# Kernel tuning notes

Hardware: AMD Instinct MI355X
Metric: run time of the kernel (lower is better)

The kernel has to match this reference:

```python
import jax, jax.numpy as jnp
import numpy as np

N_NODES = 100000
N_EDGES = 1600000
IN_DIM = 128
HID = 128
OUT = 128
NUM_GRAPHS = 2048


def setup_inputs() -> dict:
    key = jax.random.key(0)
    ks = jax.random.split(key, 10)
    x = jax.random.normal(ks[0], (N_NODES, IN_DIM), dtype=jnp.float32)
    edge_index = jax.random.randint(ks[1], (2, N_EDGES), 0, N_NODES, dtype=jnp.int32)
    graph_index = jnp.sort(jax.random.randint(ks[2], (N_NODES,), 0, NUM_GRAPHS, dtype=jnp.int32))
    def glorot(k, fi, fo):
        lim = jnp.sqrt(6.0 / (fi + fo)).astype(jnp.float32)
        return jax.random.uniform(k, (fi, fo), jnp.float32, -lim, lim)
    return {
        "x": x,
        "edge_index": edge_index,
        "graph_index": graph_index,
        "num_graphs": NUM_GRAPHS,
        "W1": glorot(ks[3], IN_DIM, HID), "b1": jnp.zeros((HID,), jnp.float32),
        "W2": glorot(ks[4], HID, HID),    "b2": jnp.zeros((HID,), jnp.float32),
        "W3": glorot(ks[5], HID, OUT),    "b3": jnp.zeros((OUT,), jnp.float32),
    }


def _gcn_layer(x, src, dst, norm, W, b, n_nodes):
    # transform first (cheap GEMM), then normalized gather-scatter aggregation
    h = x @ W                              # [N, F]
    msg = h[src] * norm[:, None]           # [E+N, F] gather + scale
    out = jax.ops.segment_sum(msg, dst, num_segments=n_nodes)  # scatter-add
    return out + b


def reference(x, edge_index, graph_index, num_graphs, W1, b1, W2, b2, W3, b3):
    n = x.shape[0]
    # add self-loops (PyG GCNConv default)
    loops = jnp.arange(n, dtype=edge_index.dtype)
    src = jnp.concatenate([edge_index[0], loops])
    dst = jnp.concatenate([edge_index[1], loops])
    # symmetric normalization D^-1/2 (A+I) D^-1/2, degree = in-degree incl. self-loop
    deg = jax.ops.segment_sum(jnp.ones_like(src, dtype=x.dtype), dst, num_segments=n)
    dinv = jax.lax.rsqrt(jnp.maximum(deg, 1.0))
    norm = dinv[src] * dinv[dst]
    # 3 conv layers + ReLU (dropout = identity at inference)
    h = jax.nn.relu(_gcn_layer(x, src, dst, norm, W1, b1, n))
    h = jax.nn.relu(_gcn_layer(h, src, dst, norm, W2, b2, n))
    h = jax.nn.relu(_gcn_layer(h, src, dst, norm, W3, b3, n))
    # global mean / max pooling per graph
    gsum = jax.ops.segment_sum(h, graph_index, num_segments=num_graphs)
    cnt = jax.ops.segment_sum(jnp.ones((n,), h.dtype), graph_index, num_segments=num_graphs)
    gmean = gsum / jnp.maximum(cnt, 1.0)[:, None]
    gmax = jax.ops.segment_max(h, graph_index, num_segments=num_graphs)
    return jnp.concatenate([gmean, gmax], axis=-1)
```

## Files before the change

### kernel.cpp

```cpp
#include <hip/hip_runtime.h>
#include <hip/hip_bf16.h>
#include <stdint.h>

#define N_NODES   100000
#define N_EDGES   1600000
#define FDIM      128
#define NUM_GR    2048
#define CSR_CAP   64

#define NBKT      391
#define BKT_CAP   4864
#define TILE      4096
#define LBIN_CAP  16
#define LBIN_STR  17

typedef __attribute__((ext_vector_type(8))) short short8;
typedef __attribute__((ext_vector_type(4))) float f32x4;

__device__ __forceinline__ uint32_t pk2(float a, float b) {
    __hip_bfloat16 x = __float2bfloat16(a), y = __float2bfloat16(b);
    uint16_t ux = *reinterpret_cast<uint16_t*>(&x);
    uint16_t uy = *reinterpret_cast<uint16_t*>(&y);
    return (uint32_t)ux | ((uint32_t)uy << 16);
}

__device__ __forceinline__ float bflo(uint32_t u) { return __uint_as_float(u << 16); }
__device__ __forceinline__ float bfhi(uint32_t u) { return __uint_as_float(u & 0xFFFF0000u); }

__device__ __forceinline__ short8 pack8(float4 u0, float4 u1) {
    union { uint32_t u[4]; short8 s; } cv;
    cv.u[0] = pk2(u0.x, u0.y);
    cv.u[1] = pk2(u0.z, u0.w);
    cv.u[2] = pk2(u1.x, u1.y);
    cv.u[3] = pk2(u1.z, u1.w);
    return cv.s;
}

__device__ __forceinline__ int lower_bound_dev(const int* a, int n, int key) {
    int lo = 0, hi = n;
    while (lo < hi) {
        int m = (lo + hi) >> 1;
        if (a[m] < key) lo = m + 1; else hi = m;
    }
    return lo;
}


__global__ __launch_bounds__(256, 4) void k_fused1(
        const float* __restrict__ x, const float* __restrict__ W1,
        __hip_bfloat16* __restrict__ C, int n, int gGemm,
        const int* __restrict__ src, const int* __restrict__ dst,
        int* __restrict__ bkt_cnt, int* __restrict__ bkt, int E, int gA,
        const float* __restrict__ W2, const float* __restrict__ W3,
        __hip_bfloat16* __restrict__ wt,
        const int* __restrict__ gidx, float* __restrict__ gscale) {
    __shared__ uint32_t smem[8192];
    const int b = blockIdx.x;
    const int tid = threadIdx.x;

    if (b >= gGemm + gA + 128) {
        int g = (b - (gGemm + gA + 128)) * 256 + tid;
        if (g < NUM_GR) {
            int lo = lower_bound_dev(gidx, n, g);
            int hi = lower_bound_dev(gidx, n, g + 1);
            gscale[g] = 1.f / (float)max(hi - lo, 1);
        }
        return;
    }

    if (b >= gGemm + gA) {
        int idx = 16384 + (b - gGemm - gA) * 256 + tid;
        int l = idx >> 14, rem = idx & 16383, c = rem >> 7, k = rem & 127;
        const float* W = (l == 1) ? W2 : W3;
        wt[idx] = __float2bfloat16(W[k * FDIM + c]);
        return;
    }

    if (b >= gGemm) {
        int* binCnt  = (int*)smem;
        int* binBase = (int*)smem + NBKT;
        int* bins    = (int*)smem + 2 * NBKT;
        int bb = b - gGemm;

        for (int i = tid; i < NBKT; i += 256) binCnt[i] = 0;
        __syncthreads();

        int e0 = bb * TILE;
        int e1 = min(E, e0 + TILE);
        for (int e = e0 + tid; e < e1; e += 256) {
            int s = src[e];
            int d = dst[e];
            int bi = d >> 8;
            int rec = ((d & 255) << 17) | s;
            int pos = atomicAdd(&binCnt[bi], 1);
            if (pos < LBIN_CAP) {
                bins[bi * LBIN_STR + pos] = rec;
            } else {
                int gp = atomicAdd(&bkt_cnt[bi], 1);
                if (gp < BKT_CAP) bkt[bi * BKT_CAP + gp] = rec;
            }
        }
        __syncthreads();

        for (int i = tid; i < NBKT; i += 256) {
            int c = min(binCnt[i], LBIN_CAP);
            binBase[i] = (c > 0) ? atomicAdd(&bkt_cnt[i], c) : 0;
        }
        __syncthreads();

        for (int i = tid; i < NBKT * LBIN_CAP; i += 256) {
            int bi = i / LBIN_CAP, sl = i - bi * LBIN_CAP;
            if (sl < min(binCnt[bi], LBIN_CAP)) {
                int gp = binBase[bi] + sl;
                if (gp < BKT_CAP) bkt[bi * BKT_CAP + gp] = bins[bi * LBIN_STR + sl];
            }
        }
        return;
    }

    uint32_t* Wtl = smem;

    const int rowBase = b * 128;

    for (int it = 0; it < 32; ++it) {
        int idx = it * 256 + tid;
        int kp = idx >> 7;
        int c  = idx & 127;
        float w0 = W1[(size_t)(2 * kp) * FDIM + c];
        float w1 = W1[(size_t)(2 * kp + 1) * FDIM + c];
        int word = c * 64 + ((((kp >> 2) ^ (c & 7)) << 2) | (kp & 3));
        Wtl[word] = pk2(w0, w1);
    }
    __syncthreads();

    const int w = tid >> 6;
    const int lane = tid & 63;
    const int r = lane & 15;
    const int q = lane >> 4;

    const int r0c = min(rowBase + w * 32 + r, n - 1);
    const int r1c = min(rowBase + w * 32 + 16 + r, n - 1);

    f32x4 acc[8][2] = {};

#pragma unroll
    for (int kk = 0; kk < 4; ++kk) {
        int co = (kk * 4 + q) * 8;
        const float4* p0 = (const float4*)&x[(size_t)r0c * FDIM + co];
        const float4* p1 = (const float4*)&x[(size_t)r1c * FDIM + co];
        short8 a0 = pack8(p0[0], p0[1]);
        short8 a1 = pack8(p1[0], p1[1]);
        int gr = ((kk * 4 + q) ^ (r & 7)) << 2;
#pragma unroll
        for (int m = 0; m < 8; ++m) {
            short8 bw = *(const short8*)&Wtl[(m * 16 + r) * 64 + gr];
            acc[m][0] = __builtin_amdgcn_mfma_f32_16x16x32_bf16(bw, a0, acc[m][0], 0, 0, 0);
            acc[m][1] = __builtin_amdgcn_mfma_f32_16x16x32_bf16(bw, a1, acc[m][1], 0, 0, 0);
        }
    }

#pragma unroll
    for (int nt = 0; nt < 2; ++nt) {
        int node = rowBase + w * 32 + nt * 16 + r;
        if (node < n) {
#pragma unroll
            for (int m = 0; m < 8; ++m) {
                f32x4 v = acc[m][nt];
                uint2 pv;
                pv.x = pk2(v[0], v[1]);
                pv.y = pk2(v[2], v[3]);
                *(uint2*)&C[(size_t)node * FDIM + m * 16 + q * 4] = pv;
            }
        }
    }
}


__global__ __launch_bounds__(256) void k_csr(const int* __restrict__ bkt_cnt,
                                             const int* __restrict__ bkt,
                                             int* __restrict__ cnt,
                                             float* __restrict__ dinv,
                                             int* __restrict__ csr, int n) {
    __shared__ int lc[64];
    __shared__ int cur[64];
    int b = blockIdx.x;
    int tid = threadIdx.x;
    int bi = b >> 2;
    int qd = b & 3;

    if (b == 0 && tid == 0) dinv[n] = 0.f;

    if (tid < 64) { lc[tid] = 0; cur[tid] = 0; }
    __syncthreads();

    int len = min(bkt_cnt[bi], BKT_CAP);
    const int* recs = bkt + bi * BKT_CAP;

    for (int i = tid; i < len; i += 256) {
        int dl = (recs[i] >> 17) & 255;
        if ((dl >> 6) == qd) atomicAdd(&lc[dl & 63], 1);
    }
    __syncthreads();

    if (tid < 64) {
        int v = (bi << 8) + (qd << 6) + tid;
        if (v < n) {
            int c = lc[tid];
            cnt[v] = c;
            dinv[v] = rsqrtf((float)(c + 1));
        }
    }

    for (int i = tid; i < len; i += 256) {
        int rec = recs[i];
        int dl = (rec >> 17) & 255;
        if ((dl >> 6) == qd) {
            int pos = atomicAdd(&cur[dl & 63], 1);
            if (pos < CSR_CAP)
                csr[(((size_t)(bi << 8) + dl) << 6) + pos] = rec & 0x1FFFF;
        }
    }
}


__global__ __launch_bounds__(256) void k_agg1(const __hip_bfloat16* __restrict__ T,
                                              const int* __restrict__ cnt,
                                              const int* __restrict__ csr,
                                              const float* __restrict__ dinv,
                                              const float* __restrict__ bias,
                                              uint32_t* __restrict__ Hb,
                                              int n) {
    int wid = (blockIdx.x * 256 + threadIdx.x) >> 6;
    int lane = threadIdx.x & 63;
    if (wid >= n) return;
    int v = wid;
    int g   = lane >> 4;
    int s16 = lane & 15;

    const uint4* Tu4 = (const uint4*)T;

    int cv  = min(cnt[v], CSR_CAP);
    int sraw = csr[((size_t)v << 6) + lane];
    int sidx = (lane < cv) ? sraw : ((lane == cv) ? v : n);
    cv += 1;

    float a0 = 0.f, a1 = 0.f, a2 = 0.f, a3 = 0.f;
    float a4 = 0.f, a5 = 0.f, a6 = 0.f, a7 = 0.f;

    int mr = (cv + 15) & ~15;
    for (int j = 0; j < mr; j += 16) {
        uint4 gg[4];
        float wv[4];
#pragma unroll
        for (int t = 0; t < 4; ++t) {
            int it = __shfl(sidx, j + 4 * t + g, 64);
            wv[t] = dinv[it];
            gg[t] = Tu4[(size_t)it * 16 + s16];
        }
#pragma unroll
        for (int t = 0; t < 4; ++t) {
            a0 = fmaf(wv[t], bflo(gg[t].x), a0); a1 = fmaf(wv[t], bfhi(gg[t].x), a1);
            a2 = fmaf(wv[t], bflo(gg[t].y), a2); a3 = fmaf(wv[t], bfhi(gg[t].y), a3);
            a4 = fmaf(wv[t], bflo(gg[t].z), a4); a5 = fmaf(wv[t], bfhi(gg[t].z), a5);
            a6 = fmaf(wv[t], bflo(gg[t].w), a6); a7 = fmaf(wv[t], bfhi(gg[t].w), a7);
        }
    }

    a0 += __shfl_xor(a0, 16, 64); a0 += __shfl_xor(a0, 32, 64);
    a1 += __shfl_xor(a1, 16, 64); a1 += __shfl_xor(a1, 32, 64);
    a2 += __shfl_xor(a2, 16, 64); a2 += __shfl_xor(a2, 32, 64);
    a3 += __shfl_xor(a3, 16, 64); a3 += __shfl_xor(a3, 32, 64);
    a4 += __shfl_xor(a4, 16, 64); a4 += __shfl_xor(a4, 32, 64);
    a5 += __shfl_xor(a5, 16, 64); a5 += __shfl_xor(a5, 32, 64);
    a6 += __shfl_xor(a6, 16, 64); a6 += __shfl_xor(a6, 32, 64);
    a7 += __shfl_xor(a7, 16, 64); a7 += __shfl_xor(a7, 32, 64);

    if (g == 0) {
        float dv = dinv[v];
        float4 bb0 = *(const float4*)&bias[s16 * 8];
        float4 bb1 = *(const float4*)&bias[s16 * 8 + 4];
        float r0 = fmaxf(fmaf(dv, a0, bb0.x), 0.f);
        float r1 = fmaxf(fmaf(dv, a1, bb0.y), 0.f);
        float r2 = fmaxf(fmaf(dv, a2, bb0.z), 0.f);
        float r3 = fmaxf(fmaf(dv, a3, bb0.w), 0.f);
        float r4 = fmaxf(fmaf(dv, a4, bb1.x), 0.f);
        float r5 = fmaxf(fmaf(dv, a5, bb1.y), 0.f);
        float r6 = fmaxf(fmaf(dv, a6, bb1.z), 0.f);
        float r7 = fmaxf(fmaf(dv, a7, bb1.w), 0.f);
        uint4 pv;
        pv.x = pk2(r0, r1);
        pv.y = pk2(r2, r3);
        pv.z = pk2(r4, r5);
        pv.w = pk2(r6, r7);
        *(uint4*)&Hb[(size_t)v * 64 + s16 * 4] = pv;
    }
}


template<int POOL>
__global__ __launch_bounds__(512, 4) void k_aggT(
        const __hip_bfloat16* __restrict__ T,
        const __hip_bfloat16* __restrict__ Wt,
        const int* __restrict__ cnt,
        const int* __restrict__ csr,
        const float* __restrict__ dinv,
        const float* __restrict__ bias,
        uint32_t* __restrict__ Hb,
        const int* __restrict__ gidx,
        const float* __restrict__ gscale,
        float* __restrict__ out,
        int n) {
    __shared__ uint32_t Wl[128 * 64];
    __shared__ uint32_t Hl[32 * 64];

    const int tid = threadIdx.x;

    for (int it = 0; it < 4; ++it) {
        int g = it * 512 + tid;
        int r = g >> 4;
        int seg = g & 15;
        uint4 v = *(const uint4*)&Wt[(size_t)r * FDIM + seg * 8];
        int word = r * 64 + ((seg ^ (r & 7)) << 2);
        *(uint4*)&Wl[word] = v;
    }

    const int w = tid >> 6;
    const int lane = tid & 63;
    const int g = lane >> 4;
    const int s16 = lane & 15;
    const int nodeBase = blockIdx.x * 32;
    const uint4* Tu4 = (const uint4*)T;

    for (int k = 0; k < 4; ++k) {
        int v = nodeBase + w * 4 + k;
        int cv = min(cnt[v], CSR_CAP);
        int sraw = csr[((size_t)v << 6) + lane];
        int sidx = (lane < cv) ? sraw : ((lane == cv) ? v : n);
        cv += 1;

        float a0 = 0.f, a1 = 0.f, a2 = 0.f, a3 = 0.f;
        float a4 = 0.f, a5 = 0.f, a6 = 0.f, a7 = 0.f;

        int mr = (cv + 15) & ~15;
        for (int j = 0; j < mr; j += 16) {
            uint4 gg[4];
            float wv[4];
#pragma unroll
            for (int t = 0; t < 4; ++t) {
                int it = __shfl(sidx, j + 4 * t + g, 64);
                wv[t] = dinv[it];
                gg[t] = Tu4[(size_t)it * 16 + s16];
            }
#pragma unroll
            for (int t = 0; t < 4; ++t) {
                a0 = fmaf(wv[t], bflo(gg[t].x), a0); a1 = fmaf(wv[t], bfhi(gg[t].x), a1);
                a2 = fmaf(wv[t], bflo(gg[t].y), a2); a3 = fmaf(wv[t], bfhi(gg[t].y), a3);
                a4 = fmaf(wv[t], bflo(gg[t].z), a4); a5 = fmaf(wv[t], bfhi(gg[t].z), a5);
                a6 = fmaf(wv[t], bflo(gg[t].w), a6); a7 = fmaf(wv[t], bfhi(gg[t].w), a7);
            }
        }

        a0 += __shfl_xor(a0, 16, 64); a0 += __shfl_xor(a0, 32, 64);
        a1 += __shfl_xor(a1, 16, 64); a1 += __shfl_xor(a1, 32, 64);
        a2 += __shfl_xor(a2, 16, 64); a2 += __shfl_xor(a2, 32, 64);
        a3 += __shfl_xor(a3, 16, 64); a3 += __shfl_xor(a3, 32, 64);
        a4 += __shfl_xor(a4, 16, 64); a4 += __shfl_xor(a4, 32, 64);
        a5 += __shfl_xor(a5, 16, 64); a5 += __shfl_xor(a5, 32, 64);
        a6 += __shfl_xor(a6, 16, 64); a6 += __shfl_xor(a6, 32, 64);
        a7 += __shfl_xor(a7, 16, 64); a7 += __shfl_xor(a7, 32, 64);

        if (g == 0) {
            float dv = dinv[v];
            int row = w * 4 + k;
            uint4 pv;
            pv.x = pk2(a0 * dv, a1 * dv);
            pv.y = pk2(a2 * dv, a3 * dv);
            pv.z = pk2(a4 * dv, a5 * dv);
            pv.w = pk2(a6 * dv, a7 * dv);
            *(uint4*)&Hl[row * 64 + ((s16 ^ (row & 7)) << 2)] = pv;
        }
    }
    __syncthreads();

    const int r = lane & 15;
    const int q = lane >> 4;

    f32x4 acc[2] = {};
#pragma unroll
    for (int kk = 0; kk < 4; ++kk) {
        int gr = ((kk * 4 + q) ^ (r & 7)) << 2;
        short8 a0 = *(const short8*)&Hl[r * 64 + gr];
        short8 a1 = *(const short8*)&Hl[(16 + r) * 64 + gr];
        short8 bw = *(const short8*)&Wl[(w * 16 + r) * 64 + gr];
        acc[0] = __builtin_amdgcn_mfma_f32_16x16x32_bf16(bw, a0, acc[0], 0, 0, 0);
        acc[1] = __builtin_amdgcn_mfma_f32_16x16x32_bf16(bw, a1, acc[1], 0, 0, 0);
    }

    float4 bb = *(const float4*)&bias[w * 16 + q * 4];

    if constexpr (!POOL) {
#pragma unroll
        for (int nt = 0; nt < 2; ++nt) {
            int node = nodeBase + nt * 16 + r;
            f32x4 vv = acc[nt];
            float r0 = fmaxf(vv[0] + bb.x, 0.f);
            float r1 = fmaxf(vv[1] + bb.y, 0.f);
            float r2 = fmaxf(vv[2] + bb.z, 0.f);
            float r3 = fmaxf(vv[3] + bb.w, 0.f);
            uint2 pv;
            pv.x = pk2(r0, r1);
            pv.y = pk2(r2, r3);
            *(uint2*)&Hb[(size_t)node * 64 + w * 8 + q * 2] = pv;
        }
    } else {
        __syncthreads();
        float* Pl = (float*)Wl;
        int* lds_g = (int*)Hl;
#pragma unroll
        for (int nt = 0; nt < 2; ++nt) {
            int row = nt * 16 + r;
            f32x4 vv = acc[nt];
            float* dstp = &Pl[row * 130 + w * 16 + q * 4];
            dstp[0] = fmaxf(vv[0] + bb.x, 0.f);
            dstp[1] = fmaxf(vv[1] + bb.y, 0.f);
            dstp[2] = fmaxf(vv[2] + bb.z, 0.f);
            dstp[3] = fmaxf(vv[3] + bb.w, 0.f);
        }
        if (tid < 32) lds_g[tid] = gidx[nodeBase + tid];
        __syncthreads();
        if (tid < 128) {
            int f = tid;
            int cg = lds_g[0];
            float s = 0.f, m = 0.f;
            for (int row = 0; row < 32; ++row) {
                int gw = lds_g[row];
                float hv = Pl[row * 130 + f];
                if (gw != cg) {
                    atomicAdd(&out[(size_t)cg * 256 + f], s * gscale[cg]);
                    atomicMax((unsigned int*)&out[(size_t)cg * 256 + 128 + f],
                              __float_as_uint(m));
                    s = 0.f; m = 0.f; cg = gw;
                }
                s += hv;
                m = fmaxf(m, hv);
            }
            atomicAdd(&out[(size_t)cg * 256 + f], s * gscale[cg]);
            atomicMax((unsigned int*)&out[(size_t)cg * 256 + 128 + f],
                      __float_as_uint(m));
        }
    }
}


extern "C" void kernel_launch(void* const* d_in, const int* in_sizes, int n_in,
                              void* d_out, int out_size, void* d_ws, size_t ws_size,
                              hipStream_t stream) {
    const float* x    = (const float*)d_in[0];
    const int*   ei   = (const int*)d_in[1];
    const int*   gidx = (const int*)d_in[2];
    const float* W1 = (const float*)d_in[4];
    const float* b1 = (const float*)d_in[5];
    const float* W2 = (const float*)d_in[6];
    const float* b2 = (const float*)d_in[7];
    const float* W3 = (const float*)d_in[8];
    const float* b3 = (const float*)d_in[9];
    float* out = (float*)d_out;

    const int N = N_NODES, E = N_EDGES;
    const int* src = ei;
    const int* dst = ei + E;

    char* ws = (char*)d_ws;
    size_t o = 0;
    auto alloc = [&](size_t bytes) { size_t r = o; o += (bytes + 255) & ~(size_t)255; return r; };
    size_t o_bktcnt = alloc((size_t)NBKT * 4);
    size_t o_bkt    = alloc((size_t)NBKT * BKT_CAP * 4);
    size_t o_cnt    = alloc((size_t)N * 4);
    size_t o_dinv   = alloc((size_t)(N + 1) * 4);
    size_t o_csr    = alloc((size_t)NBKT * 256 * CSR_CAP * 4);
    size_t o_wt     = alloc((size_t)3 * FDIM * FDIM * 2);
    size_t o_ta     = alloc((size_t)(N + 1) * FDIM * 2);
    size_t o_tb     = alloc((size_t)(N + 1) * FDIM * 2);
    size_t o_gs     = alloc((size_t)NUM_GR * 4);

    int*   bkt_cnt = (int*)(ws + o_bktcnt);
    int*   bkt     = (int*)(ws + o_bkt);
    int*   cnt     = (int*)(ws + o_cnt);
    float* dinv    = (float*)(ws + o_dinv);
    int*   csr     = (int*)(ws + o_csr);
    __hip_bfloat16* wtbuf = (__hip_bfloat16*)(ws + o_wt);
    __hip_bfloat16* bufA  = (__hip_bfloat16*)(ws + o_ta);
    __hip_bfloat16* bufB  = (__hip_bfloat16*)(ws + o_tb);
    float* gscale = (float*)(ws + o_gs);

    hipMemsetAsync(bkt_cnt, 0, (size_t)NBKT * 4, stream);
    hipMemsetAsync(bufA + (size_t)N * FDIM, 0, FDIM * 2, stream);
    hipMemsetAsync(bufB + (size_t)N * FDIM, 0, FDIM * 2, stream);
    hipMemsetAsync(out, 0, (size_t)NUM_GR * 2 * FDIM * 4, stream);

    const int gA    = (E + TILE - 1) / TILE;
    const int gGemm = (N + 127) / 128;

    k_fused1<<<gGemm + gA + 128 + 8, 256, 0, stream>>>(x, W1, bufA, N, gGemm,
                                                       src, dst, bkt_cnt, bkt, E, gA,
                                                       W2, W3, wtbuf, gidx, gscale);
    k_csr<<<NBKT * 4, 256, 0, stream>>>(bkt_cnt, bkt, cnt, dinv, csr, N);

    k_agg1<<<(N + 3) / 4, 256, 0, stream>>>(bufA, cnt, csr, dinv, b1,
                                            (uint32_t*)bufB, N);
    k_aggT<0><<<N / 32, 512, 0, stream>>>(bufB, wtbuf + FDIM * FDIM,
                                          cnt, csr, dinv, b2, (uint32_t*)bufA,
                                          nullptr, nullptr, nullptr, N);
    k_aggT<1><<<N / 32, 512, 0, stream>>>(bufA, wtbuf + 2 * FDIM * FDIM,
                                          cnt, csr, dinv, b3, nullptr,
                                          gidx, gscale, out, N);
}
```

Before: 368.6 us.

## Build CSR via direct global atomics, merge prep memsets into one kernel, retile layer-2 GEMM

Drops the two-pass bucket sort with LDS binning and the k_csr kernel, and builds the padded CSR directly with a global atomicAdd per edge on each destination's counter. A small k_prep kernel then computes dinv and zeroes the padding rows and the output, replacing three memsets. The non-pooling aggregation+GEMM path is restructured so each wave computes 4 rows across all 128 output columns, with the sync moved to before aggregation. The design removes an extra pass over edges and one launch, at the cost of heavily contended, scattered global atomics and writes.

Result: slower. 427.1 us (+15.9%).

```diff
diff --git a/kernel.cpp b/kernel.cpp
--- a/kernel.cpp
+++ b/kernel.cpp
@@ -7,12 +7,8 @@
 #define FDIM      128
 #define NUM_GR    2048
 #define CSR_CAP   64
-
-#define NBKT      391
-#define BKT_CAP   4864
+#define NPAD      100096
 #define TILE      4096
-#define LBIN_CAP  16
-#define LBIN_STR  17
 
 typedef __attribute__((ext_vector_type(8))) short short8;
 typedef __attribute__((ext_vector_type(4))) float f32x4;
@@ -50,7 +46,7 @@
         const float* __restrict__ x, const float* __restrict__ W1,
         __hip_bfloat16* __restrict__ C, int n, int gGemm,
         const int* __restrict__ src, const int* __restrict__ dst,
-        int* __restrict__ bkt_cnt, int* __restrict__ bkt, int E, int gA,
+        int* __restrict__ cnt, int* __restrict__ csr, int E, int gA,
         const float* __restrict__ W2, const float* __restrict__ W3,
         __hip_bfloat16* __restrict__ wt,
         const int* __restrict__ gidx, float* __restrict__ gscale) {
@@ -77,43 +73,14 @@
     }
 
     if (b >= gGemm) {
-        int* binCnt  = (int*)smem;
-        int* binBase = (int*)smem + NBKT;
-        int* bins    = (int*)smem + 2 * NBKT;
         int bb = b - gGemm;
-
-        for (int i = tid; i < NBKT; i += 256) binCnt[i] = 0;
-        __syncthreads();
-
         int e0 = bb * TILE;
         int e1 = min(E, e0 + TILE);
         for (int e = e0 + tid; e < e1; e += 256) {
             int s = src[e];
             int d = dst[e];
-            int bi = d >> 8;
-            int rec = ((d & 255) << 17) | s;
-            int pos = atomicAdd(&binCnt[bi], 1);
-            if (pos < LBIN_CAP) {
-                bins[bi * LBIN_STR + pos] = rec;
-            } else {
-                int gp = atomicAdd(&bkt_cnt[bi], 1);
-                if (gp < BKT_CAP) bkt[bi * BKT_CAP + gp] = rec;
-            }
-        }
-        __syncthreads();
-
-        for (int i = tid; i < NBKT; i += 256) {
-            int c = min(binCnt[i], LBIN_CAP);
-            binBase[i] = (c > 0) ? atomicAdd(&bkt_cnt[i], c) : 0;
-        }
-        __syncthreads();
-
-        for (int i = tid; i < NBKT * LBIN_CAP; i += 256) {
-            int bi = i / LBIN_CAP, sl = i - bi * LBIN_CAP;
-            if (sl < min(binCnt[bi], LBIN_CAP)) {
-                int gp = binBase[bi] + sl;
-                if (gp < BKT_CAP) bkt[bi * BKT_CAP + gp] = bins[bi * LBIN_STR + sl];
-            }
+            int pos = atomicAdd(&cnt[d], 1);
+            if (pos < CSR_CAP) csr[((size_t)d << 6) + pos] = s;
         }
         return;
     }
@@ -176,50 +143,19 @@
 }
 
 
-__global__ __launch_bounds__(256) void k_csr(const int* __restrict__ bkt_cnt,
-                                             const int* __restrict__ bkt,
-                                             int* __restrict__ cnt,
-                                             float* __restrict__ dinv,
-                                             int* __restrict__ csr, int n) {
-    __shared__ int lc[64];
-    __shared__ int cur[64];
-    int b = blockIdx.x;
-    int tid = threadIdx.x;
-    int bi = b >> 2;
-    int qd = b & 3;
-
-    if (b == 0 && tid == 0) dinv[n] = 0.f;
-
-    if (tid < 64) { lc[tid] = 0; cur[tid] = 0; }
-    __syncthreads();
-
-    int len = min(bkt_cnt[bi], BKT_CAP);
-    const int* recs = bkt + bi * BKT_CAP;
-
-    for (int i = tid; i < len; i += 256) {
-        int dl = (recs[i] >> 17) & 255;
-        if ((dl >> 6) == qd) atomicAdd(&lc[dl & 63], 1);
-    }
-    __syncthreads();
-
-    if (tid < 64) {
-        int v = (bi << 8) + (qd << 6) + tid;
-        if (v < n) {
-            int c = lc[tid];
-            cnt[v] = c;
-            dinv[v] = rsqrtf((float)(c + 1));
-        }
-    }
-
-    for (int i = tid; i < len; i += 256) {
-        int rec = recs[i];
-        int dl = (rec >> 17) & 255;
-        if ((dl >> 6) == qd) {
-            int pos = atomicAdd(&cur[dl & 63], 1);
-            if (pos < CSR_CAP)
-                csr[(((size_t)(bi << 8) + dl) << 6) + pos] = rec & 0x1FFFF;
-        }
-    }
+__global__ __launch_bounds__(256) void k_prep(const int* __restrict__ cnt,
+                                              float* __restrict__ dinv,
+                                              uint32_t* __restrict__ za,
+                                              uint32_t* __restrict__ zb,
+                                              float* __restrict__ outz, int n) {
+    int b = blockIdx.x, tid = threadIdx.x;
+    int idx = b * 256 + tid;
+    for (int i = idx; i < n; i += 65536)
+        dinv[i] = rsqrtf((float)(cnt[i] + 1));
+    if (idx == 0) dinv[n] = 0.f;
+    if (b == 0 && tid < 64) za[(size_t)n * 64 + tid] = 0;
+    if (b == 1 && tid < 64) zb[(size_t)n * 64 + tid] = 0;
+    for (int i = idx; i < NUM_GR * 256; i += 65536) outz[i] = 0.f;
 }
 
 
@@ -323,6 +259,7 @@
         int word = r * 64 + ((seg ^ (r & 7)) << 2);
         *(uint4*)&Wl[word] = v;
     }
+    __syncthreads();
 
     const int w = tid >> 6;
     const int lane = tid & 63;
@@ -380,39 +317,56 @@
             *(uint4*)&Hl[row * 64 + ((s16 ^ (row & 7)) << 2)] = pv;
         }
     }
-    __syncthreads();
 
     const int r = lane & 15;
     const int q = lane >> 4;
 
-    f32x4 acc[2] = {};
-#pragma unroll
-    for (int kk = 0; kk < 4; ++kk) {
-        int gr = ((kk * 4 + q) ^ (r & 7)) << 2;
-        short8 a0 = *(const short8*)&Hl[r * 64 + gr];
-        short8 a1 = *(const short8*)&Hl[(16 + r) * 64 + gr];
-        short8 bw = *(const short8*)&Wl[(w * 16 + r) * 64 + gr];
-        acc[0] = __builtin_amdgcn_mfma_f32_16x16x32_bf16(bw, a0, acc[0], 0, 0, 0);
-        acc[1] = __builtin_amdgcn_mfma_f32_16x16x32_bf16(bw, a1, acc[1], 0, 0, 0);
-    }
-
-    float4 bb = *(const float4*)&bias[w * 16 + q * 4];
-
     if constexpr (!POOL) {
-#pragma unroll
-        for (int nt = 0; nt < 2; ++nt) {
-            int node = nodeBase + nt * 16 + r;
-            f32x4 vv = acc[nt];
-            float r0 = fmaxf(vv[0] + bb.x, 0.f);
-            float r1 = fmaxf(vv[1] + bb.y, 0.f);
-            float r2 = fmaxf(vv[2] + bb.z, 0.f);
-            float r3 = fmaxf(vv[3] + bb.w, 0.f);
-            uint2 pv;
-            pv.x = pk2(r0, r1);
-            pv.y = pk2(r2, r3);
-            *(uint2*)&Hb[(size_t)node * 64 + w * 8 + q * 2] = pv;
+        const int row = w * 4 + (r & 3);
+        const int rs = row & 7;
+        short8 av[4];
+#pragma unroll
+        for (int kk = 0; kk < 4; ++kk)
+            av[kk] = *(const short8*)&Hl[row * 64 + (((kk * 4 + q) ^ rs) << 2)];
+
+#pragma unroll
+        for (int m = 0; m < 8; ++m) {
+            f32x4 acc = {};
+#pragma unroll
+            for (int kk = 0; kk < 4; ++kk) {
+                int gr = ((kk * 4 + q) ^ (r & 7)) << 2;
+                short8 bw = *(const short8*)&Wl[(m * 16 + r) * 64 + gr];
+                acc = __builtin_amdgcn_mfma_f32_16x16x32_bf16(bw, av[kk], acc, 0, 0, 0);
+            }
+            if (r < 4) {
+                int node = nodeBase + w * 4 + r;
+                float4 bb = *(const float4*)&bias[m * 16 + q * 4];
+                float r0 = fmaxf(acc[0] + bb.x, 0.f);
+                float r1 = fmaxf(acc[1] + bb.y, 0.f);
+                float r2 = fmaxf(acc[2] + bb.z, 0.f);
+                float r3 = fmaxf(acc[3] + bb.w, 0.f);
+                uint2 pv;
+                pv.x = pk2(r0, r1);
+                pv.y = pk2(r2, r3);
+                *(uint2*)&Hb[(size_t)node * 64 + m * 8 + q * 2] = pv;
+            }
         }
     } else {
+        __syncthreads();
+
+        f32x4 acc[2] = {};
+#pragma unroll
+        for (int kk = 0; kk < 4; ++kk) {
+            int gr = ((kk * 4 + q) ^ (r & 7)) << 2;
+            short8 a0 = *(const short8*)&Hl[r * 64 + gr];
+            short8 a1 = *(const short8*)&Hl[(16 + r) * 64 + gr];
+            short8 bw = *(const short8*)&Wl[(w * 16 + r) * 64 + gr];
+            acc[0] = __builtin_amdgcn_mfma_f32_16x16x32_bf16(bw, a0, acc[0], 0, 0, 0);
+            acc[1] = __builtin_amdgcn_mfma_f32_16x16x32_bf16(bw, a1, acc[1], 0, 0, 0);
+        }
+
+        float4 bb = *(const float4*)&bias[w * 16 + q * 4];
+
         __syncthreads();
         float* Pl = (float*)Wl;
         int* lds_g = (int*)Hl;
@@ -473,18 +427,14 @@
     char* ws = (char*)d_ws;
     size_t o = 0;
     auto alloc = [&](size_t bytes) { size_t r = o; o += (bytes + 255) & ~(size_t)255; return r; };
-    size_t o_bktcnt = alloc((size_t)NBKT * 4);
-    size_t o_bkt    = alloc((size_t)NBKT * BKT_CAP * 4);
     size_t o_cnt    = alloc((size_t)N * 4);
     size_t o_dinv   = alloc((size_t)(N + 1) * 4);
-    size_t o_csr    = alloc((size_t)NBKT * 256 * CSR_CAP * 4);
+    size_t o_csr    = alloc((size_t)NPAD * CSR_CAP * 4);
     size_t o_wt     = alloc((size_t)3 * FDIM * FDIM * 2);
     size_t o_ta     = alloc((size_t)(N + 1) * FDIM * 2);
     size_t o_tb     = alloc((size_t)(N + 1) * FDIM * 2);
     size_t o_gs     = alloc((size_t)NUM_GR * 4);
 
-    int*   bkt_cnt = (int*)(ws + o_bktcnt);
-    int*   bkt     = (int*)(ws + o_bkt);
     int*   cnt     = (int*)(ws + o_cnt);
     float* dinv    = (float*)(ws + o_dinv);
     int*   csr     = (int*)(ws + o_csr);
@@ -493,18 +443,16 @@
     __hip_bfloat16* bufB  = (__hip_bfloat16*)(ws + o_tb);
     float* gscale = (float*)(ws + o_gs);
 
-    hipMemsetAsync(bkt_cnt, 0, (size_t)NBKT * 4, stream);
-    hipMemsetAsync(bufA + (size_t)N * FDIM, 0, FDIM * 2, stream);
-    hipMemsetAsync(bufB + (size_t)N * FDIM, 0, FDIM * 2, stream);
-    hipMemsetAsync(out, 0, (size_t)NUM_GR * 2 * FDIM * 4, stream);
+    hipMemsetAsync(cnt, 0, (size_t)N * 4, stream);
 
     const int gA    = (E + TILE - 1) / TILE;
     const int gGemm = (N + 127) / 128;
 
     k_fused1<<<gGemm + gA + 128 + 8, 256, 0, stream>>>(x, W1, bufA, N, gGemm,
-                                                       src, dst, bkt_cnt, bkt, E, gA,
+                                                       src, dst, cnt, csr, E, gA,
                                                        W2, W3, wtbuf, gidx, gscale);
-    k_csr<<<NBKT * 4, 256, 0, stream>>>(bkt_cnt, bkt, cnt, dinv, csr, N);
+    k_prep<<<256, 256, 0, stream>>>(cnt, dinv, (uint32_t*)bufA, (uint32_t*)bufB,
+                                    out, N);
 
     k_agg1<<<(N + 3) / 4, 256, 0, stream>>>(bufA, cnt, csr, dinv, b1,
                                             (uint32_t*)bufB, N);
```
